# Optimization experiments

Hardware: AMD Instinct MI355X
Metric: run time of the kernel (lower is better)

## Reference

```python
import jax, jax.numpy as jnp
import numpy as np

N_NODES = 100000
EPS = 1e-5


def _layernorm(x, gamma, beta):
    mu = jnp.mean(x, axis=-1, keepdims=True)
    var = jnp.mean(jnp.square(x - mu), axis=-1, keepdims=True)
    return (x - mu) * jax.lax.rsqrt(var + EPS) * gamma + beta


def _gcn_layer(src, dst, feat, gamma, beta, W, b):
    # copy_u + sum: aggregate source features into destination nodes
    agg = jax.ops.segment_sum(feat[src], dst, num_segments=N_NODES)
    h = _layernorm(agg, gamma, beta)
    return h @ W + b


def setup_inputs() -> dict:
    key = jax.random.key(0)
    ks = jax.random.split(key, 16)
    d_in, d_hid, d_out = 128, 128, 128
    E = 1600000

    def lin(k, fan_in, fan_out):
        kw, kb = jax.random.split(k)
        lim = 1.0 / np.sqrt(fan_in)
        W = jax.random.uniform(kw, (fan_in, fan_out), jnp.float32, -lim, lim)
        b = jax.random.uniform(kb, (fan_out,), jnp.float32, -lim, lim)
        return W, b

    W1, b1 = lin(ks[0], d_in, d_hid)
    W2, b2 = lin(ks[1], d_hid, d_hid)
    W3, b3 = lin(ks[2], d_hid, d_out)
    return {
        "features": jax.random.normal(ks[3], (N_NODES, d_in), jnp.float32),
        "src": jax.random.randint(ks[4], (E,), 0, N_NODES, jnp.int32),
        "dst": jax.random.randint(ks[5], (E,), 0, N_NODES, jnp.int32),
        "g1": jnp.ones((d_in,), jnp.float32), "be1": jnp.zeros((d_in,), jnp.float32),
        "W1": W1, "b1": b1,
        "g2": jnp.ones((d_hid,), jnp.float32), "be2": jnp.zeros((d_hid,), jnp.float32),
        "W2": W2, "b2": b2,
        "g3": jnp.ones((d_hid,), jnp.float32), "be3": jnp.zeros((d_hid,), jnp.float32),
        "W3": W3, "b3": b3,
    }


def reference(features, src, dst, g1, be1, W1, b1, g2, be2, W2, b2, g3, be3, W3, b3):
    x = jax.nn.relu(_gcn_layer(src, dst, features, g1, be1, W1, b1))
    x = jax.nn.relu(_gcn_layer(src, dst, x, g2, be2, W2, b2))
    x = _gcn_layer(src, dst, x, g3, be3, W3, b3)
    return x
```

## Files before the change

### kernel.cpp

```cpp
#include <hip/hip_runtime.h>
#include <hip/hip_bf16.h>
#include <stdint.h>

typedef unsigned short u16;
typedef __attribute__((ext_vector_type(8))) short short8;
typedef __attribute__((ext_vector_type(4))) float f32x4;

#define DIM 128
#define CAP 64

__device__ __forceinline__ float bflo(uint32_t v) {
    uint32_t b = v << 16;
    float f; __builtin_memcpy(&f, &b, 4); return f;
}
__device__ __forceinline__ float bfhi(uint32_t v) {
    uint32_t b = v & 0xffff0000u;
    float f; __builtin_memcpy(&f, &b, 4); return f;
}
__device__ __forceinline__ u16 f2bf(float f) {
    uint32_t x; __builtin_memcpy(&x, &f, 4);
    uint32_t r = (x + 0x7fffu + ((x >> 16) & 1u)) >> 16;
    return (u16)r;
}
__device__ __forceinline__ uint32_t pack2bf(float a, float b) {
    return (uint32_t)f2bf(a) | ((uint32_t)f2bf(b) << 16);
}


__global__ __launch_bounds__(256) void k_bin1(
    const int* __restrict__ src, const int* __restrict__ dst,
    uint32_t* __restrict__ gCur, uint32_t* __restrict__ groupBuf,
    int E, int ngrp, int gcap)
{
    __shared__ uint32_t hcnt[512];
    __shared__ uint32_t hbase[512];
    __shared__ uint32_t hcur[512];
    int nb = gridDim.x;
    int per = (E + nb - 1) / nb;
    int lo = blockIdx.x * per;
    int hi = lo + per; if (hi > E) hi = E;

    for (int t = threadIdx.x; t < ngrp; t += 256) { hcnt[t] = 0; hcur[t] = 0; }
    __syncthreads();

    for (int i = lo + threadIdx.x; i < hi; i += 256)
        atomicAdd(&hcnt[((uint32_t)dst[i]) >> 8], 1u);
    __syncthreads();

    int rot = (blockIdx.x * 37) % (ngrp > 0 ? ngrp : 1);
    for (int k = threadIdx.x; k < ngrp; k += 256) {
        int t = k + rot; if (t >= ngrp) t -= ngrp;
        uint32_t c = hcnt[t];
        hbase[t] = c ? atomicAdd(&gCur[t], c) : 0u;
    }
    __syncthreads();

    for (int i = lo + threadIdx.x; i < hi; i += 256) {
        uint32_t d = (uint32_t)dst[i];
        uint32_t g = d >> 8;
        uint32_t off = hbase[g] + atomicAdd(&hcur[g], 1u);
        if (off < (uint32_t)gcap)
            groupBuf[(size_t)g * gcap + off] = (uint32_t)src[i] | ((d & 255u) << 20);
    }
}

__global__ __launch_bounds__(256) void k_bin2(
    const uint32_t* __restrict__ groupBuf, const uint32_t* __restrict__ gCur,
    uint32_t* __restrict__ bucket, uint32_t* __restrict__ cnt,
    int N, int gcap)
{
    __shared__ uint32_t ncur[256];
    int g = blockIdx.x;
    ncur[threadIdx.x] = 0;
    __syncthreads();
    uint32_t m = gCur[g]; if (m > (uint32_t)gcap) m = gcap;
    int nodebase = g << 8;
    const uint32_t* buf = groupBuf + (size_t)g * gcap;
    for (uint32_t i = threadIdx.x; i < m; i += 256) {
        uint32_t v = buf[i];
        uint32_t nl = v >> 20;
        uint32_t s = v & 0xFFFFFu;
        uint32_t pos = atomicAdd(&ncur[nl], 1u);
        if (pos < CAP) bucket[(size_t)(nodebase + (int)nl) * CAP + pos] = s;
    }
    __syncthreads();
    int node = nodebase + threadIdx.x;
    if (node < N) cnt[node] = ncur[threadIdx.x];
}


__global__ void k_prep(const float* __restrict__ feat, uint32_t* __restrict__ X0,
                       uint32_t* __restrict__ X, int N,
                       const float* __restrict__ W1, const float* __restrict__ W2,
                       const float* __restrict__ W3,
                       u16* __restrict__ t0, u16* __restrict__ t1, u16* __restrict__ t2)
{
    int b = blockIdx.x;
    if (b < 3) {
        const float* w = b == 0 ? W1 : (b == 1 ? W2 : W3);
        u16* o = b == 0 ? t0 : (b == 1 ? t1 : t2);
        for (int idx = threadIdx.x; idx < DIM * DIM; idx += blockDim.x) {
            int r = idx >> 7, c = idx & 127;
            o[c * DIM + r] = f2bf(w[idx]);
        }
    } else if (b == 3) {
        int t = threadIdx.x;
        if (t < 64) X0[(size_t)N * 64 + t] = 0u;
        else if (t < 128) X[(size_t)N * 64 + (t - 64)] = 0u;
    } else {
        int n4 = N * 32;
        int i = (b - 4) * 256 + threadIdx.x;
        int stride = (gridDim.x - 4) * 256;
        const float4* in4 = (const float4*)feat;
        uint2* out2 = (uint2*)X0;
        for (; i < n4; i += stride) {
            float4 v = in4[i];
            uint2 r;
            r.x = pack2bf(v.x, v.y);
            r.y = pack2bf(v.z, v.w);
            out2[i] = r;
        }
    }
}


__global__ __launch_bounds__(256) void k_gather_ln(
    const uint32_t* __restrict__ xin, const uint32_t* __restrict__ cnt,
    const uint32_t* __restrict__ bucket,
    const int* __restrict__ src, const int* __restrict__ dst,
    const float* __restrict__ gamma, const float* __restrict__ beta,
    uint32_t* __restrict__ h, int N, int E)
{
    int w = threadIdx.x >> 6, l = threadIdx.x & 63;
    int node0 = __builtin_amdgcn_readfirstlane(2 * (blockIdx.x * 4 + w));
    if (node0 >= N) return;
    int node1 = node0 + 1;
    bool has1 = node1 < N;
    uint32_t c0 = cnt[node0];
    uint32_t c1 = has1 ? cnt[node1] : 0u;
    float a0 = 0.f, a1 = 0.f, b0 = 0.f, b1 = 0.f;

    if (__builtin_expect(c0 > CAP || c1 > CAP, 0)) {
        for (int e = 0; e < E; ++e) {
            int d = dst[e];
            if (d == node0) { uint32_t v = xin[(size_t)src[e] * 64 + l]; a0 += bflo(v); a1 += bfhi(v); }
            else if (d == node1) { uint32_t v = xin[(size_t)src[e] * 64 + l]; b0 += bflo(v); b1 += bfhi(v); }
        }
    } else {
        {
            uint32_t bktv = bucket[(size_t)node0 * CAP + l];
#pragma unroll
            for (int g = 0; g < 4; ++g) {
                if ((uint32_t)(g * 16) < c0) {
                    uint32_t v[16];
#pragma unroll
                    for (int i = 0; i < 16; ++i) {
                        const int SLOT = g * 16 + i;
                        uint32_t su = (uint32_t)__builtin_amdgcn_readfirstlane(
                            (int)((uint32_t)__builtin_amdgcn_readlane(bktv, SLOT)));
                        su = ((uint32_t)SLOT < c0) ? su : (uint32_t)N;
                        v[i] = (xin + (size_t)su * 64)[l];
                    }
#pragma unroll
                    for (int i = 0; i < 16; ++i) { a0 += bflo(v[i]); a1 += bfhi(v[i]); }
                }
            }
        }
        if (has1) {
            uint32_t bktv = bucket[(size_t)node1 * CAP + l];
#pragma unroll
            for (int g = 0; g < 4; ++g) {
                if ((uint32_t)(g * 16) < c1) {
                    uint32_t v[16];
#pragma unroll
                    for (int i = 0; i < 16; ++i) {
                        const int SLOT = g * 16 + i;
                        uint32_t su = (uint32_t)__builtin_amdgcn_readfirstlane(
                            (int)((uint32_t)__builtin_amdgcn_readlane(bktv, SLOT)));
                        su = ((uint32_t)SLOT < c1) ? su : (uint32_t)N;
                        v[i] = (xin + (size_t)su * 64)[l];
                    }
#pragma unroll
                    for (int i = 0; i < 16; ++i) { b0 += bflo(v[i]); b1 += bfhi(v[i]); }
                }
            }
        }
    }

    float sA = a0 + a1, qA = a0 * a0 + a1 * a1;
    float sB = b0 + b1, qB = b0 * b0 + b1 * b1;
    for (int off = 32; off; off >>= 1) {
        sA += __shfl_xor(sA, off, 64);
        sB += __shfl_xor(sB, off, 64);
        qA += __shfl_xor(qA, off, 64);
        qB += __shfl_xor(qB, off, 64);
    }
    float gg0 = gamma[2 * l], gg1 = gamma[2 * l + 1];
    float bb0 = beta[2 * l],  bb1 = beta[2 * l + 1];
    {
        float mean = sA * (1.f / 128.f);
        float var  = qA * (1.f / 128.f) - mean * mean;
        float rs   = rsqrtf(var + 1e-5f);
        h[(size_t)node0 * 64 + l] =
            pack2bf((a0 - mean) * rs * gg0 + bb0, (a1 - mean) * rs * gg1 + bb1);
    }
    if (has1) {
        float mean = sB * (1.f / 128.f);
        float var  = qB * (1.f / 128.f) - mean * mean;
        float rs   = rsqrtf(var + 1e-5f);
        h[(size_t)node1 * 64 + l] =
            pack2bf((b0 - mean) * rs * gg0 + bb0, (b1 - mean) * rs * gg1 + bb1);
    }
}


template <int RELU, int OUTF32>
__global__ __launch_bounds__(256) void k_gemm(
    const u16* __restrict__ h, const u16* __restrict__ wt,
    const float* __restrict__ bias, void* __restrict__ outp, int N)
{
    int w = threadIdx.x >> 6, l = threadIdx.x & 63;
    int colbase = (w >> 1) * 64;
    int lr = l & 15, lg = l >> 4;

    short8 bfrag[4][4];
    float bv[4];
#pragma unroll
    for (int ct = 0; ct < 4; ++ct) {
        bv[ct] = bias[colbase + ct * 16 + lr];
#pragma unroll
        for (int kc = 0; kc < 4; ++kc)
            bfrag[ct][kc] = *(const short8*)(wt + (size_t)(colbase + ct * 16 + lr) * DIM + kc * 32 + lg * 8);
    }

    int ntiles = (N + 31) / 32;
    int t = blockIdx.x;
    if (t >= ntiles) return;

    auto loadA = [&](int tt, short8* af) {
        int ar = tt * 32 + 16 * (w & 1) + lr;
        if (ar > N - 1) ar = N - 1;
#pragma unroll
        for (int kc = 0; kc < 4; ++kc)
            af[kc] = *(const short8*)(h + (size_t)ar * DIM + kc * 32 + lg * 8);
    };

    short8 afrag[4];
    loadA(t, afrag);

    while (true) {
        int tn = t + (int)gridDim.x;
        bool has = tn < ntiles;
        short8 anext[4];
        if (has) loadA(tn, anext);

        int row0 = t * 32 + 16 * (w & 1);
#pragma unroll
        for (int ct = 0; ct < 4; ++ct) {
            f32x4 a = {0.f, 0.f, 0.f, 0.f};
#pragma unroll
            for (int kc = 0; kc < 4; ++kc)
                a = __builtin_amdgcn_mfma_f32_16x16x32_bf16(afrag[kc], bfrag[ct][kc], a, 0, 0, 0);
            int col = colbase + ct * 16 + lr;
#pragma unroll
            for (int j = 0; j < 4; ++j) {
                int row = row0 + lg * 4 + j;
                float v = a[j] + bv[ct];
                if (RELU) v = fmaxf(v, 0.f);
                if (row < N) {
                    if (OUTF32) ((float*)outp)[(size_t)row * DIM + col] = v;
                    else        ((u16*)outp)[(size_t)row * DIM + col] = f2bf(v);
                }
            }
        }

        if (!has) break;
#pragma unroll
        for (int kc = 0; kc < 4; ++kc) afrag[kc] = anext[kc];
        t = tn;
    }
}


extern "C" void kernel_launch(void* const* d_in, const int* in_sizes, int n_in,
                              void* d_out, int out_size, void* d_ws, size_t ws_size,
                              hipStream_t stream) {
    const float* feat = (const float*)d_in[0];
    const int* src  = (const int*)d_in[1];
    const int* dst  = (const int*)d_in[2];
    const float* g1 = (const float*)d_in[3],  *be1 = (const float*)d_in[4];
    const float* W1 = (const float*)d_in[5],  *b1  = (const float*)d_in[6];
    const float* g2 = (const float*)d_in[7],  *be2 = (const float*)d_in[8];
    const float* W2 = (const float*)d_in[9],  *b2  = (const float*)d_in[10];
    const float* g3 = (const float*)d_in[11], *be3 = (const float*)d_in[12];
    const float* W3 = (const float*)d_in[13], *b3  = (const float*)d_in[14];

    int N = in_sizes[0] / DIM;
    int E = in_sizes[1];
    float* out = (float*)d_out;

    int ngrp = (N + 255) >> 8;
    int gcap = (E / (ngrp > 0 ? ngrp : 1)) * 3 / 2 + 1024;
    int npair = (N + 1) / 2;

    char* ws = (char*)d_ws;
    auto alloc = [&](size_t bytes) {
        char* p = ws;
        ws += (bytes + 255) & ~(size_t)255;
        return p;
    };
    uint32_t* gCur     = (uint32_t*)alloc((size_t)ngrp * 4);
    uint32_t* groupBuf = (uint32_t*)alloc((size_t)ngrp * gcap * 4);
    uint32_t* cnt      = (uint32_t*)alloc((size_t)N * 4);
    uint32_t* bucket   = (uint32_t*)alloc((size_t)N * CAP * 4);
    u16* wt1 = (u16*)alloc(DIM * DIM * 2);
    u16* wt2 = (u16*)alloc(DIM * DIM * 2);
    u16* wt3 = (u16*)alloc(DIM * DIM * 2);
    uint32_t* X0 = (uint32_t*)alloc((size_t)(N + 1) * 64 * 4);
    uint32_t* H  = (uint32_t*)alloc((size_t)(N + 1) * 64 * 4);
    uint32_t* X  = (uint32_t*)alloc((size_t)(N + 1) * 64 * 4);

    hipMemsetAsync(gCur, 0, (size_t)ngrp * 4, stream);
    k_bin1<<<512, 256, 0, stream>>>(src, dst, gCur, groupBuf, E, ngrp, gcap);
    k_bin2<<<ngrp, 256, 0, stream>>>(groupBuf, gCur, bucket, cnt, N, gcap);
    k_prep<<<1028, 256, 0, stream>>>(feat, X0, X, N, W1, W2, W3, wt1, wt2, wt3);

    int gblocks = (npair + 3) / 4;

    k_gather_ln<<<gblocks, 256, 0, stream>>>(X0, cnt, bucket, src, dst, g1, be1, H, N, E);
    k_gemm<1, 0><<<512, 256, 0, stream>>>((const u16*)H, wt1, b1, X, N);
    k_gather_ln<<<gblocks, 256, 0, stream>>>(X, cnt, bucket, src, dst, g2, be2, H, N, E);
    k_gemm<1, 0><<<512, 256, 0, stream>>>((const u16*)H, wt2, b2, X, N);
    k_gather_ln<<<gblocks, 256, 0, stream>>>(X, cnt, bucket, src, dst, g3, be3, H, N, E);
    k_gemm<0, 1><<<512, 256, 0, stream>>>((const u16*)H, wt3, b3, out, N);
}
```

Baseline: 305.4 us.

## Fuse gather-layernorm with MFMA GEMM per 16-node tile via LDS

```diff
diff --git a/kernel.cpp b/kernel.cpp
--- a/kernel.cpp
+++ b/kernel.cpp
@@ -8,6 +8,7 @@
 
 #define DIM 128
 #define CAP 64
+#define LROW 68
 
 __device__ __forceinline__ float bflo(uint32_t v) {
     uint32_t b = v << 16;
@@ -90,7 +91,7 @@
 
 
 __global__ void k_prep(const float* __restrict__ feat, uint32_t* __restrict__ X0,
-                       uint32_t* __restrict__ X, int N,
+                       uint32_t* __restrict__ X1, uint32_t* __restrict__ X2, int N,
                        const float* __restrict__ W1, const float* __restrict__ W2,
                        const float* __restrict__ W3,
                        u16* __restrict__ t0, u16* __restrict__ t1, u16* __restrict__ t2)
@@ -105,8 +106,9 @@
         }
     } else if (b == 3) {
         int t = threadIdx.x;
-        if (t < 64) X0[(size_t)N * 64 + t] = 0u;
-        else if (t < 128) X[(size_t)N * 64 + (t - 64)] = 0u;
+        if (t < 64)       X0[(size_t)N * 64 + t] = 0u;
+        else if (t < 128) X1[(size_t)N * 64 + (t - 64)] = 0u;
+        else if (t < 192) X2[(size_t)N * 64 + (t - 128)] = 0u;
     } else {
         int n4 = N * 32;
         int i = (b - 4) * 256 + threadIdx.x;
@@ -124,20 +126,25 @@
 }
 
 
-__global__ __launch_bounds__(256) void k_gather_ln(
+template <int RELU, int OUTF32>
+__global__ __launch_bounds__(512) void k_fused(
     const uint32_t* __restrict__ xin, const uint32_t* __restrict__ cnt,
     const uint32_t* __restrict__ bucket,
     const int* __restrict__ src, const int* __restrict__ dst,
     const float* __restrict__ gamma, const float* __restrict__ beta,
-    uint32_t* __restrict__ h, int N, int E)
+    const u16* __restrict__ wt, const float* __restrict__ bias,
+    void* __restrict__ outp, int N, int E)
 {
+    __shared__ uint32_t lds[16 * LROW];
     int w = threadIdx.x >> 6, l = threadIdx.x & 63;
-    int node0 = __builtin_amdgcn_readfirstlane(2 * (blockIdx.x * 4 + w));
-    if (node0 >= N) return;
+    int base = blockIdx.x * 16;
+
+    int node0 = __builtin_amdgcn_readfirstlane(base + 2 * w);
     int node1 = node0 + 1;
-    bool has1 = node1 < N;
-    uint32_t c0 = cnt[node0];
-    uint32_t c1 = has1 ? cnt[node1] : 0u;
+    int n0c = node0 < N ? node0 : N - 1;
+    int n1c = node1 < N ? node1 : N - 1;
+    uint32_t c0 = (node0 < N) ? cnt[n0c] : 0u;
+    uint32_t c1 = (node1 < N) ? cnt[n1c] : 0u;
     float a0 = 0.f, a1 = 0.f, b0 = 0.f, b1 = 0.f;
 
     if (__builtin_expect(c0 > CAP || c1 > CAP, 0)) {
@@ -148,7 +155,7 @@
         }
     } else {
         {
-            uint32_t bktv = bucket[(size_t)node0 * CAP + l];
+            uint32_t bktv = bucket[(size_t)n0c * CAP + l];
 #pragma unroll
             for (int g = 0; g < 4; ++g) {
                 if ((uint32_t)(g * 16) < c0) {
@@ -166,8 +173,8 @@
                 }
             }
         }
-        if (has1) {
-            uint32_t bktv = bucket[(size_t)node1 * CAP + l];
+        {
+            uint32_t bktv = bucket[(size_t)n1c * CAP + l];
 #pragma unroll
             for (int g = 0; g < 4; ++g) {
                 if ((uint32_t)(g * 16) < c1) {
@@ -201,83 +208,47 @@
         float mean = sA * (1.f / 128.f);
         float var  = qA * (1.f / 128.f) - mean * mean;
         float rs   = rsqrtf(var + 1e-5f);
-        h[(size_t)node0 * 64 + l] =
+        lds[(2 * w) * LROW + l] =
             pack2bf((a0 - mean) * rs * gg0 + bb0, (a1 - mean) * rs * gg1 + bb1);
     }
-    if (has1) {
+    {
         float mean = sB * (1.f / 128.f);
         float var  = qB * (1.f / 128.f) - mean * mean;
         float rs   = rsqrtf(var + 1e-5f);
-        h[(size_t)node1 * 64 + l] =
+        lds[(2 * w + 1) * LROW + l] =
             pack2bf((b0 - mean) * rs * gg0 + bb0, (b1 - mean) * rs * gg1 + bb1);
     }
-}
-
-
-template <int RELU, int OUTF32>
-__global__ __launch_bounds__(256) void k_gemm(
-    const u16* __restrict__ h, const u16* __restrict__ wt,
-    const float* __restrict__ bias, void* __restrict__ outp, int N)
-{
-    int w = threadIdx.x >> 6, l = threadIdx.x & 63;
-    int colbase = (w >> 1) * 64;
+    __syncthreads();
+
     int lr = l & 15, lg = l >> 4;
-
-    short8 bfrag[4][4];
-    float bv[4];
-#pragma unroll
-    for (int ct = 0; ct < 4; ++ct) {
-        bv[ct] = bias[colbase + ct * 16 + lr];
-#pragma unroll
-        for (int kc = 0; kc < 4; ++kc)
-            bfrag[ct][kc] = *(const short8*)(wt + (size_t)(colbase + ct * 16 + lr) * DIM + kc * 32 + lg * 8);
-    }
-
-    int ntiles = (N + 31) / 32;
-    int t = blockIdx.x;
-    if (t >= ntiles) return;
-
-    auto loadA = [&](int tt, short8* af) {
-        int ar = tt * 32 + 16 * (w & 1) + lr;
-        if (ar > N - 1) ar = N - 1;
-#pragma unroll
-        for (int kc = 0; kc < 4; ++kc)
-            af[kc] = *(const short8*)(h + (size_t)ar * DIM + kc * 32 + lg * 8);
-    };
+    const u16* ldsu = (const u16*)lds;
 
     short8 afrag[4];
-    loadA(t, afrag);
-
-    while (true) {
-        int tn = t + (int)gridDim.x;
-        bool has = tn < ntiles;
-        short8 anext[4];
-        if (has) loadA(tn, anext);
-
-        int row0 = t * 32 + 16 * (w & 1);
-#pragma unroll
-        for (int ct = 0; ct < 4; ++ct) {
-            f32x4 a = {0.f, 0.f, 0.f, 0.f};
-#pragma unroll
-            for (int kc = 0; kc < 4; ++kc)
-                a = __builtin_amdgcn_mfma_f32_16x16x32_bf16(afrag[kc], bfrag[ct][kc], a, 0, 0, 0);
-            int col = colbase + ct * 16 + lr;
-#pragma unroll
-            for (int j = 0; j < 4; ++j) {
-                int row = row0 + lg * 4 + j;
-                float v = a[j] + bv[ct];
-                if (RELU) v = fmaxf(v, 0.f);
-                if (row < N) {
-                    if (OUTF32) ((float*)outp)[(size_t)row * DIM + col] = v;
-                    else        ((u16*)outp)[(size_t)row * DIM + col] = f2bf(v);
-                }
-            }
-        }
-
-        if (!has) break;
-#pragma unroll
-        for (int kc = 0; kc < 4; ++kc) afrag[kc] = anext[kc];
-        t = tn;
+#pragma unroll
+    for (int kc = 0; kc < 4; ++kc)
+        afrag[kc] = *(const short8*)&ldsu[lr * (LROW * 2) + kc * 32 + lg * 8];
+
+    int col = w * 16 + lr;
+    short8 bfrag[4];
+#pragma unroll
+    for (int kc = 0; kc < 4; ++kc)
+        bfrag[kc] = *(const short8*)(wt + (size_t)col * DIM + kc * 32 + lg * 8);
+
+    f32x4 acc = {0.f, 0.f, 0.f, 0.f};
+#pragma unroll
+    for (int kc = 0; kc < 4; ++kc)
+        acc = __builtin_amdgcn_mfma_f32_16x16x32_bf16(afrag[kc], bfrag[kc], acc, 0, 0, 0);
+
+    float bv = bias[col];
+#pragma unroll
+    for (int j = 0; j < 4; ++j) {
+        int row = base + lg * 4 + j;
+        float v = acc[j] + bv;
+        if (RELU) v = fmaxf(v, 0.f);
+        if (row < N) {
+            if (OUTF32) ((float*)outp)[(size_t)row * DIM + col] = v;
+            else        ((u16*)outp)[(size_t)row * DIM + col] = f2bf(v);
+        }
     }
 }
 
@@ -301,7 +272,6 @@
 
     int ngrp = (N + 255) >> 8;
     int gcap = (E / (ngrp > 0 ? ngrp : 1)) * 3 / 2 + 1024;
-    int npair = (N + 1) / 2;
 
     char* ws = (char*)d_ws;
     auto alloc = [&](size_t bytes) {
@@ -317,20 +287,17 @@
     u16* wt2 = (u16*)alloc(DIM * DIM * 2);
     u16* wt3 = (u16*)alloc(DIM * DIM * 2);
     uint32_t* X0 = (uint32_t*)alloc((size_t)(N + 1) * 64 * 4);
-    uint32_t* H  = (uint32_t*)alloc((size_t)(N + 1) * 64 * 4);
-    uint32_t* X  = (uint32_t*)alloc((size_t)(N + 1) * 64 * 4);
+    uint32_t* X1 = (uint32_t*)alloc((size_t)(N + 1) * 64 * 4);
+    uint32_t* X2 = (uint32_t*)alloc((size_t)(N + 1) * 64 * 4);
 
     hipMemsetAsync(gCur, 0, (size_t)ngrp * 4, stream);
     k_bin1<<<512, 256, 0, stream>>>(src, dst, gCur, groupBuf, E, ngrp, gcap);
     k_bin2<<<ngrp, 256, 0, stream>>>(groupBuf, gCur, bucket, cnt, N, gcap);
-    k_prep<<<1028, 256, 0, stream>>>(feat, X0, X, N, W1, W2, W3, wt1, wt2, wt3);
-
-    int gblocks = (npair + 3) / 4;
-
-    k_gather_ln<<<gblocks, 256, 0, stream>>>(X0, cnt, bucket, src, dst, g1, be1, H, N, E);
-    k_gemm<1, 0><<<512, 256, 0, stream>>>((const u16*)H, wt1, b1, X, N);
-    k_gather_ln<<<gblocks, 256, 0, stream>>>(X, cnt, bucket, src, dst, g2, be2, H, N, E);
-    k_gemm<1, 0><<<512, 256, 0, stream>>>((const u16*)H, wt2, b2, X, N);
-    k_gather_ln<<<gblocks, 256, 0, stream>>>(X, cnt, bucket, src, dst, g3, be3, H, N, E);
-    k_gemm<0, 1><<<512, 256, 0, stream>>>((const u16*)H, wt3, b3, out, N);
-}
+    k_prep<<<1028, 256, 0, stream>>>(feat, X0, X1, X2, N, W1, W2, W3, wt1, wt2, wt3);
+
+    int fblocks = (N + 15) / 16;
+
+    k_fused<1, 0><<<fblocks, 512, 0, stream>>>(X0, cnt, bucket, src, dst, g1, be1, wt1, b1, X1,  N, E);
+    k_fused<1, 0><<<fblocks, 512, 0, stream>>>(X1, cnt, bucket, src, dst, g2, be2, wt2, b2, X2,  N, E);
+    k_fused<0, 1><<<fblocks, 512, 0, stream>>>(X2, cnt, bucket, src, dst, g3, be3, wt3, b3, out, N, E);
+}
```

New measurement: 291.4 us. -4.6%, faster.
